# Performance work log

Measured on AMD Instinct MI355X. Metric: run time of the kernel, lower is better.

The kernel has to match this reference:

```python
import jax, jax.numpy as jnp
import numpy as np

B, T = 2048, 200
UC, IC, CC = 100000, 100000, 1000
UD, ID, CD = 128, 64, 64
K = ID + CD                      # keys_dim = item_dim + cate_dim = 128
D_JOIN = UD + K + K              # user_emb + item_join_emb + hist_hid_emb
D1, D2 = 80, 40                  # dim_layers[:-1]
BN_EPS = 1e-3                    # keras BatchNormalization default epsilon
MASK_VAL = -2.0**32 + 1.0


def _bn_train(x, gamma, beta):
    # keras BatchNorm, training mode (batch statistics over axis 0)
    m = jnp.mean(x, axis=0)
    v = jnp.var(x, axis=0)
    return (x - m) * jax.lax.rsqrt(v + BN_EPS) * gamma + beta


def _dice(x, alpha, beta):
    # dice: BN(center=False, scale=False) then learned soft gating
    m = jnp.mean(x, axis=0)
    v = jnp.var(x, axis=0)
    xn = (x - m) * jax.lax.rsqrt(v + BN_EPS)
    p = jax.nn.sigmoid(beta * xn)
    return alpha * (1.0 - p) * x + p * x


def setup_inputs() -> dict:
    key = jax.random.key(0)
    ks = jax.random.split(key, 32)
    f = jnp.float32
    inp = {
        "user": jax.random.randint(ks[0], (B,), 0, UC, dtype=jnp.int32),
        "item": jax.random.randint(ks[1], (B,), 0, IC, dtype=jnp.int32),
        "history": jax.random.randint(ks[2], (B, T), 0, IC, dtype=jnp.int32),
        "length": jax.random.randint(ks[3], (B,), 1, T + 1, dtype=jnp.int32),
        "cate_list": jax.random.randint(ks[4], (IC,), 0, CC, dtype=jnp.int32),
        # embedding tables + item bias
        "user_table": jax.random.normal(ks[5], (UC, UD), f) * 0.05,
        "item_table": jax.random.normal(ks[6], (IC, ID), f) * 0.05,
        "cate_table": jax.random.normal(ks[7], (CC, CD), f) * 0.05,
        "item_bias": jax.random.normal(ks[8], (IC,), f) * 0.01,
        # attention MLP: 4K -> 80 -> 40 -> 1 (sigmoid, sigmoid, linear)
        "att_W1": jax.random.normal(ks[9], (4 * K, D1), f) * 0.05,
        "att_b1": jnp.zeros((D1,), f),
        "att_W2": jax.random.normal(ks[10], (D1, D2), f) * 0.1,
        "att_b2": jnp.zeros((D2,), f),
        "att_W3": jax.random.normal(ks[11], (D2, 1), f) * 0.1,
        "att_b3": jnp.zeros((1,), f),
        # hist_bn + hist_fc (K -> K)
        "hbn_gamma": jnp.ones((K,), f),
        "hbn_beta": jnp.zeros((K,), f),
        "hist_W": jax.random.normal(ks[12], (K, K), f) * 0.05,
        "hist_b": jnp.zeros((K,), f),
        # final MLP: BN -> Dense(80)+dice -> Dense(40)+dice -> Dense(1)
        "fbn_gamma": jnp.ones((D_JOIN,), f),
        "fbn_beta": jnp.zeros((D_JOIN,), f),
        "fc1_W": jax.random.normal(ks[13], (D_JOIN, D1), f) * 0.05,
        "fc1_b": jnp.zeros((D1,), f),
        "d1_alpha": jax.random.normal(ks[14], (D1,), f) * 0.1,
        "d1_beta": jax.random.normal(ks[15], (D1,), f) * 0.1,
        "fc2_W": jax.random.normal(ks[16], (D1, D2), f) * 0.1,
        "fc2_b": jnp.zeros((D2,), f),
        "d2_alpha": jax.random.normal(ks[17], (D2,), f) * 0.1,
        "d2_beta": jax.random.normal(ks[18], (D2,), f) * 0.1,
        "fc3_W": jax.random.normal(ks[19], (D2, 1), f) * 0.1,
        "fc3_b": jnp.zeros((1,), f),
    }
    return inp


def reference(user, item, history, length, cate_list,
              user_table, item_table, cate_table, item_bias,
              att_W1, att_b1, att_W2, att_b2, att_W3, att_b3,
              hbn_gamma, hbn_beta, hist_W, hist_b,
              fbn_gamma, fbn_beta,
              fc1_W, fc1_b, d1_alpha, d1_beta,
              fc2_W, fc2_b, d2_alpha, d2_beta,
              fc3_W, fc3_b):
    # --- get_emb ---
    user_emb = user_table[user]                                   # [B, UD]
    item_join = jnp.concatenate([item_table[item], cate_table[cate_list[item]]], -1)  # [B, K]
    bias = item_bias[item]                                        # [B]
    hist_join = jnp.concatenate([item_table[history], cate_table[cate_list[history]]], -1)  # [B, T, K]

    # --- DIN attention ---
    q = jnp.broadcast_to(item_join[:, None, :], hist_join.shape)  # [B, T, K]
    din_all = jnp.concatenate([q, hist_join, q - hist_join, q * hist_join], -1)  # [B, T, 4K]
    h = jax.nn.sigmoid(din_all @ att_W1 + att_b1)
    h = jax.nn.sigmoid(h @ att_W2 + att_b2)
    scores = (h @ att_W3 + att_b3)[..., 0]                        # [B, T]
    mask = jnp.arange(T) < length[:, None]                        # [B, T]
    scores = jnp.where(mask, scores, MASK_VAL)
    scores = scores / (K ** 0.5)
    attn = jax.nn.softmax(scores, axis=-1)                        # [B, T]
    hist_attn = jnp.einsum('bt,btk->bk', attn, hist_join)         # [B, K]

    # --- hist_bn + hist_fc ---
    hist_hid = _bn_train(hist_attn, hbn_gamma, hbn_beta) @ hist_W + hist_b  # [B, K]

    # --- final MLP with dice ---
    join = jnp.concatenate([user_emb, item_join, hist_hid], -1)   # [B, D_JOIN]
    x = _bn_train(join, fbn_gamma, fbn_beta)
    x = _dice(x @ fc1_W + fc1_b, d1_alpha, d1_beta)
    x = _dice(x @ fc2_W + fc2_b, d2_alpha, d2_beta)
    output = (x @ fc3_W + fc3_b)[:, 0] + bias                     # [B]
    logit = jax.nn.sigmoid(output)
    return output, logit
```

## Files before the change

kernel.cpp:

```cpp
#include <hip/hip_runtime.h>
#include <math.h>

#define BB 2048
#define TT 200
#define BN_EPS 1e-3f
#define MASKV (-4294967295.0f)
#define INV_SQRTK 0.08838834764831845f

typedef short bfrag __attribute__((ext_vector_type(8)));
typedef float f32x4 __attribute__((ext_vector_type(4)));

__device__ __forceinline__ unsigned short f2b(float x) {
    union { float f; unsigned u; } v; v.f = x;
    unsigned r = (v.u + 0x7fffu + ((v.u >> 16) & 1u)) >> 16;
    return (unsigned short)r;
}
__device__ __forceinline__ float b2f(unsigned short u) {
    union { unsigned u; float f; } v; v.u = ((unsigned)u) << 16; return v.f;
}
__device__ __forceinline__ float sigm(float x) { return 1.f / (1.f + __expf(-x)); }

__global__ __launch_bounds__(256) void k0_prep(
    const float* __restrict__ W1, const float* __restrict__ fc1W,
    const float* __restrict__ fc2W, float* __restrict__ prep)
{
    const int gid = blockIdx.x * 256 + threadIdx.x;
    const int stride = gridDim.x * 256;
    float* W1bcT = prep;
    float* W1dT  = prep + 10240;
    float* W1ac  = prep + 20480;
    float* fc1WT = prep + 30720;
    float* fc2WT = prep + 61440;
    for (int i = gid; i < 10240; i += stride) {
        int j = i >> 7, k = i & 127;
        float wa = W1[k * 80 + j];
        float wb = W1[(128 + k) * 80 + j];
        float wc = W1[(256 + k) * 80 + j];
        float wd = W1[(384 + k) * 80 + j];
        W1bcT[i] = wb - wc;
        W1dT[i]  = wd;
        W1ac[k * 80 + j] = wa + wc;
    }
    for (int i = gid; i < 30720; i += stride) { int j = i / 384, c = i - j * 384; fc1WT[i] = fc1W[c * 80 + j]; }
    for (int i = gid; i < 3200;  i += stride) { int j = i / 80,  c = i - j * 80;  fc2WT[i] = fc2W[c * 40 + j]; }
}

__global__ __launch_bounds__(512) void k1_attn(
    const int* __restrict__ item, const int* __restrict__ history,
    const int* __restrict__ length, const int* __restrict__ cate_list,
    const float* __restrict__ item_table, const float* __restrict__ cate_table,
    const float* __restrict__ W1bcT, const float* __restrict__ W1dT,
    const float* __restrict__ W1ac,
    const float* __restrict__ b1, const float* __restrict__ W2,
    const float* __restrict__ b2, const float* __restrict__ W3,
    const float* __restrict__ b3,
    float* __restrict__ hist_attn, float* __restrict__ hstats)
{
    __shared__ unsigned short sA[208 * 136];
    __shared__ unsigned short sU[208 * 104];
    __shared__ unsigned short sW2[48 * 104];
    __shared__ float sQ[128], sCc[80], sCp[480], sPd[1024], sScore[256];
    __shared__ float sB2[48], sW3f[48];
    __shared__ int   sHist[TT], sCid[TT];
    __shared__ float sRed[8], sMS[2], sB3s;

    const int b   = blockIdx.x;
    const int tid = threadIdx.x;
    const int it  = item[b];
    const int len = length[b];

    if (tid < 64)       sQ[tid] = item_table[(size_t)it * 64 + tid];
    else if (tid < 128) sQ[tid] = cate_table[(size_t)cate_list[it] * 64 + (tid - 64)];
    if (tid < TT) { int h = history[(size_t)b * TT + tid]; sHist[tid] = h; sCid[tid] = cate_list[h]; }
    if (tid < 48) { sB2[tid] = (tid < 40) ? b2[tid] : 0.f; sW3f[tid] = (tid < 40) ? W3[tid] : 0.f; }
    if (tid < 256) sScore[tid] = 0.f;
    if (tid == 0) sB3s = b3[0];
    for (int i = tid; i < 8 * 136; i += 512) sA[200 * 136 + i] = 0;
    for (int i = tid; i < 48 * 104; i += 512) {
        int n = i / 104, k = i - n * 104;
        float v = (n < 40 && k < 80) ? W2[k * 40 + n] : 0.f;
        sW2[i] = f2b(v);
    }
    __syncthreads();

    for (int i = tid; i < 10240; i += 512) {
        int k = i & 127;
        sU[(i >> 7) * 136 + k] = f2b(W1bcT[i] + sQ[k] * W1dT[i]);
    }
    if (tid < 480) {
        int g = tid / 80, j = tid - g * 80;
        int kb = g * 22, ke = (kb + 22 < 128) ? kb + 22 : 128;
        float c = 0.f;
        for (int k = kb; k < ke; ++k) c = fmaf(sQ[k], W1ac[k * 80 + j], c);
        sCp[tid] = c;
    }
    for (int u = tid; u < 800; u += 512) {
        int r = u >> 2, s = u & 3;
        const float* src = (s < 2) ? (item_table + (size_t)sHist[r] * 64 + s * 32)
                                   : (cate_table + (size_t)sCid[r] * 64 + (s - 2) * 32);
        unsigned short* dst = &sA[r * 136 + s * 32];
#pragma unroll
        for (int q4 = 0; q4 < 8; ++q4) {
            float4 v = ((const float4*)src)[q4];
            ushort4 o; o.x = f2b(v.x); o.y = f2b(v.y); o.z = f2b(v.z); o.w = f2b(v.w);
            *(ushort4*)(dst + q4 * 4) = o;
        }
    }
    __syncthreads();

    if (tid < 80) {
        float c = b1[tid];
#pragma unroll
        for (int g = 0; g < 6; ++g) c += sCp[g * 80 + tid];
        sCc[tid] = c;
    }

    const int w = tid >> 6, l = tid & 63, lo16 = l & 15, hi = l >> 4;
    f32x4 accP[9];
#pragma unroll
    for (int pp = 0; pp < 9; ++pp) {
        int p = w + pp * 8;
        if (p < 65) {
            int mt = p / 5, nt = p - mt * 5;
            const unsigned short* Ab = &sA[(mt * 16 + lo16) * 136 + hi * 8];
            const unsigned short* Bb = &sU[(nt * 16 + lo16) * 136 + hi * 8];
            f32x4 acc = {0.f, 0.f, 0.f, 0.f};
#pragma unroll
            for (int ks = 0; ks < 4; ++ks) {
                bfrag a = *(const bfrag*)(Ab + ks * 32);
                bfrag bb = *(const bfrag*)(Bb + ks * 32);
                acc = __builtin_amdgcn_mfma_f32_16x16x32_bf16(a, bb, acc, 0, 0, 0);
            }
            accP[pp] = acc;
        }
    }
    __syncthreads();

#pragma unroll
    for (int pp = 0; pp < 9; ++pp) {
        int p = w + pp * 8;
        if (p < 65) {
            int mt = p / 5, nt = p - mt * 5;
            int j = nt * 16 + lo16;
            float cc = sCc[j];
#pragma unroll
            for (int rg = 0; rg < 4; ++rg) {
                int m = mt * 16 + hi * 4 + rg;
                sU[m * 104 + j] = f2b(sigm(accP[pp][rg] + cc));
            }
        }
    }
    for (int i = tid; i < 208 * 16; i += 512) {
        int r = i >> 4;
        sU[r * 104 + 80 + (i & 15)] = 0;
    }
    __syncthreads();

#pragma unroll
    for (int pp = 0; pp < 5; ++pp) {
        int p = w + pp * 8;
        if (p < 39) {
            int mt = p / 3, nt = p - mt * 3;
            const unsigned short* Ab = &sU[(mt * 16 + lo16) * 104 + hi * 8];
            const unsigned short* Bb = &sW2[(nt * 16 + lo16) * 104 + hi * 8];
            f32x4 acc = {0.f, 0.f, 0.f, 0.f};
#pragma unroll
            for (int ks = 0; ks < 3; ++ks) {
                bfrag a = *(const bfrag*)(Ab + ks * 32);
                bfrag bb = *(const bfrag*)(Bb + ks * 32);
                acc = __builtin_amdgcn_mfma_f32_16x16x32_bf16(a, bb, acc, 0, 0, 0);
            }
            int j2 = nt * 16 + lo16;
            float w3 = sW3f[j2], b2v = sB2[j2];
#pragma unroll
            for (int rg = 0; rg < 4; ++rg) {
                float pt = sigm(acc[rg] + b2v) * w3;
                pt += __shfl_xor(pt, 1);
                pt += __shfl_xor(pt, 2);
                pt += __shfl_xor(pt, 4);
                pt += __shfl_xor(pt, 8);
                if (lo16 == 0) atomicAdd(&sScore[mt * 16 + hi * 4 + rg], pt);
            }
        }
    }
    __syncthreads();

    int t = tid;
    float sc;
    if (t < TT) {
        float raw = sScore[t] + sB3s;
        if (t >= len) raw = MASKV;
        sc = raw * INV_SQRTK;
    } else {
        sc = -3.0e38f;
    }
    float mx = sc;
#pragma unroll
    for (int o = 32; o > 0; o >>= 1) mx = fmaxf(mx, __shfl_xor(mx, o));
    if ((tid & 63) == 0) sRed[tid >> 6] = mx;
    __syncthreads();
    if (tid == 0) {
        float m2 = sRed[0];
        for (int ww = 1; ww < 8; ++ww) m2 = fmaxf(m2, sRed[ww]);
        sMS[0] = m2;
    }
    __syncthreads();
    mx = sMS[0];
    float e = (t < TT) ? __expf(sc - mx) : 0.f;
    float sum = e;
#pragma unroll
    for (int o = 32; o > 0; o >>= 1) sum += __shfl_xor(sum, o);
    if ((tid & 63) == 0) sRed[tid >> 6] = sum;
    __syncthreads();
    if (tid == 0) {
        float s2 = 0.f;
        for (int ww = 0; ww < 8; ++ww) s2 += sRed[ww];
        sMS[1] = s2;
    }
    __syncthreads();
    float inv = 1.f / sMS[1];
    if (t < TT) sScore[t] = e * inv;
    __syncthreads();

    {
        const int k2 = (tid & 63) * 2;
        const int g  = tid >> 6;
        float a0 = 0.f, a1 = 0.f;
        for (int tt = g; tt < TT; tt += 8) {
            float aw = sScore[tt];
            unsigned pr = *(const unsigned*)&sA[tt * 136 + k2];
            a0 = fmaf(aw, b2f((unsigned short)(pr & 0xffffu)), a0);
            a1 = fmaf(aw, b2f((unsigned short)(pr >> 16)), a1);
        }
        sPd[g * 128 + k2]     = a0;
        sPd[g * 128 + k2 + 1] = a1;
    }
    __syncthreads();
    if (tid < 128) {
        float tot = 0.f;
#pragma unroll
        for (int g = 0; g < 8; ++g) tot += sPd[g * 128 + tid];
        hist_attn[(size_t)b * 128 + tid] = tot;
        atomicAdd(&hstats[tid], tot);
        atomicAdd(&hstats[128 + tid], tot * tot);
    }
}

__global__ __launch_bounds__(256) void k3_histfc_join(
    const float* __restrict__ hist_attn, const float* __restrict__ hstats,
    const float* __restrict__ hgamma, const float* __restrict__ hbeta,
    const float* __restrict__ histW, const float* __restrict__ histb,
    const int* __restrict__ user, const int* __restrict__ item,
    const int* __restrict__ cate_list,
    const float* __restrict__ user_table, const float* __restrict__ item_table,
    const float* __restrict__ cate_table,
    float* __restrict__ jbuf, float* __restrict__ jstats)
{
    __shared__ float sWs[128][132];
    __shared__ float sX[8][132];
    __shared__ float sCsP[2][128];
    __shared__ float sCb[128];
    __shared__ float sScale[128];
    __shared__ float sShift[128];

    const int tid = threadIdx.x;
    const int r0  = blockIdx.x * 8;
    if (tid < 128) {
        float m  = hstats[tid] * (1.f / 2048.f);
        float v  = hstats[128 + tid] * (1.f / 2048.f) - m * m;
        float rs = rsqrtf(v + BN_EPS);
        float scv = hgamma[tid] * rs;
        sScale[tid] = scv;
        sShift[tid] = hbeta[tid] - m * scv;
        sCb[tid] = histb[tid];
    }
    __syncthreads();
    for (int i = tid; i < 128 * 128; i += 256) {
        int k = i >> 7;
        sWs[k][i & 127] = sScale[k] * histW[i];
    }
    {
        int j = tid & 127, g = tid >> 7;
        float c = 0.f;
        for (int k = g * 64; k < g * 64 + 64; ++k) c = fmaf(sShift[k], histW[k * 128 + j], c);
        sCsP[g][j] = c;
    }
    for (int i = tid; i < 8 * 128; i += 256) {
        int r = i >> 7;
        sX[r][i & 127] = hist_attn[(size_t)(r0 + r) * 128 + (i & 127)];
    }
    __syncthreads();

    const int j  = tid & 127;
    const int rh = tid >> 7;
    float su0 = 0.f, su1 = 0.f, su2 = 0.f, sq0 = 0.f, sq1 = 0.f, sq2 = 0.f;
    for (int r = rh; r < 8; r += 2) {
        int row = r0 + r;
        float o = sCsP[0][j] + sCsP[1][j] + sCb[j];
        for (int k = 0; k < 128; ++k) o = fmaf(sX[r][k], sWs[k][j], o);
        int u    = user[row];
        float ue = user_table[(size_t)u * 128 + j];
        int itv  = item[row];
        float qv = (j < 64) ? item_table[(size_t)itv * 64 + j]
                            : cate_table[(size_t)cate_list[itv] * 64 + (j - 64)];
        jbuf[(size_t)row * 384 + j]       = ue;
        jbuf[(size_t)row * 384 + 128 + j] = qv;
        jbuf[(size_t)row * 384 + 256 + j] = o;
        su0 += ue; sq0 = fmaf(ue, ue, sq0);
        su1 += qv; sq1 = fmaf(qv, qv, sq1);
        su2 += o;  sq2 = fmaf(o, o, sq2);
    }
    atomicAdd(&jstats[j], su0);            atomicAdd(&jstats[384 + j], sq0);
    atomicAdd(&jstats[128 + j], su1);      atomicAdd(&jstats[384 + 128 + j], sq1);
    atomicAdd(&jstats[256 + j], su2);      atomicAdd(&jstats[384 + 256 + j], sq2);
}

__global__ __launch_bounds__(256) void k4_fc1(
    const float* __restrict__ jbuf, const float* __restrict__ jstats,
    const float* __restrict__ fgamma, const float* __restrict__ fbeta,
    const float* __restrict__ fc1WT, const float* __restrict__ fc1b,
    float* __restrict__ pre1, float* __restrict__ p1stats)
{
    __shared__ float sXn[8][388];
    __shared__ float sScale[384];
    __shared__ float sShift[384];
    const int tid = threadIdx.x;
    const int r0  = blockIdx.x * 8;
    for (int c = tid; c < 384; c += 256) {
        float m  = jstats[c] * (1.f / 2048.f);
        float v  = jstats[384 + c] * (1.f / 2048.f) - m * m;
        float rs = rsqrtf(v + BN_EPS);
        float scv = fgamma[c] * rs;
        sScale[c] = scv;
        sShift[c] = fbeta[c] - m * scv;
    }
    __syncthreads();
    for (int i = tid; i < 8 * 384; i += 256) {
        int r = i / 384, c = i - r * 384;
        sXn[r][c] = jbuf[(size_t)(r0 + r) * 384 + c] * sScale[c] + sShift[c];
    }
    __syncthreads();
    const int j1 = tid % 80;
    const int rg = tid / 80;
    if (rg < 3) {
        const float* wrow = fc1WT + (size_t)j1 * 384;
        float bias = fc1b[j1];
        float su = 0.f, sq = 0.f;
        for (int r = rg; r < 8; r += 3) {
            float a = bias;
            for (int c = 0; c < 384; c += 4) {
                float4 wv = *(const float4*)(wrow + c);
                float4 xv = *(const float4*)&sXn[r][c];
                a = fmaf(wv.x, xv.x, fmaf(wv.y, xv.y, fmaf(wv.z, xv.z, fmaf(wv.w, xv.w, a))));
            }
            pre1[(size_t)(r0 + r) * 80 + j1] = a;
            su += a;
            sq = fmaf(a, a, sq);
        }
        atomicAdd(&p1stats[j1], su);
        atomicAdd(&p1stats[80 + j1], sq);
    }
}

__global__ __launch_bounds__(256) void k5_fc2(
    const float* __restrict__ pre1, const float* __restrict__ p1stats,
    const float* __restrict__ d1a, const float* __restrict__ d1b,
    const float* __restrict__ fc2WT, const float* __restrict__ fc2b,
    float* __restrict__ pre2, float* __restrict__ p2stats)
{
    __shared__ float sX1[8][84];
    __shared__ float sM[80], sRs[80], sA[80], sBt[80];
    const int tid = threadIdx.x;
    const int r0  = blockIdx.x * 8;
    if (tid < 80) {
        float m = p1stats[tid] * (1.f / 2048.f);
        float v = p1stats[80 + tid] * (1.f / 2048.f) - m * m;
        sM[tid]  = m;
        sRs[tid] = rsqrtf(v + BN_EPS);
        sA[tid]  = d1a[tid];
        sBt[tid] = d1b[tid];
    }
    __syncthreads();
    for (int i = tid; i < 8 * 80; i += 256) {
        int r = i / 80, c = i - r * 80;
        float x  = pre1[(size_t)(r0 + r) * 80 + c];
        float xn = (x - sM[c]) * sRs[c];
        float p  = sigm(sBt[c] * xn);
        sX1[r][c] = x * (p + sA[c] * (1.f - p));
    }
    __syncthreads();
    const int j2 = tid % 40;
    const int rg = tid / 40;
    if (rg < 6) {
        const float* wrow = fc2WT + (size_t)j2 * 80;
        float bias = fc2b[j2];
        float su = 0.f, sq = 0.f;
        for (int r = rg; r < 8; r += 6) {
            float a = bias;
            for (int c = 0; c < 80; c += 4) {
                float4 wv = *(const float4*)(wrow + c);
                float4 xv = *(const float4*)&sX1[r][c];
                a = fmaf(wv.x, xv.x, fmaf(wv.y, xv.y, fmaf(wv.z, xv.z, fmaf(wv.w, xv.w, a))));
            }
            pre2[(size_t)(r0 + r) * 40 + j2] = a;
            su += a;
            sq = fmaf(a, a, sq);
        }
        atomicAdd(&p2stats[j2], su);
        atomicAdd(&p2stats[40 + j2], sq);
    }
}

__global__ __launch_bounds__(256) void k6_out(
    const float* __restrict__ pre2, const float* __restrict__ p2stats,
    const float* __restrict__ d2a, const float* __restrict__ d2b,
    const float* __restrict__ fc3W, const float* __restrict__ fc3b,
    const float* __restrict__ item_bias, const int* __restrict__ item,
    float* __restrict__ outp)
{
    __shared__ float sP[256 * 41];
    __shared__ float sM[40], sRs[40], sA[40], sBt[40], sW[40];
    __shared__ float sB3v;
    const int tid = threadIdx.x;
    const int r0  = blockIdx.x * 256;
    if (tid < 40) {
        float m = p2stats[tid] * (1.f / 2048.f);
        float v = p2stats[40 + tid] * (1.f / 2048.f) - m * m;
        sM[tid]  = m;
        sRs[tid] = rsqrtf(v + BN_EPS);
        sA[tid]  = d2a[tid];
        sBt[tid] = d2b[tid];
        sW[tid]  = fc3W[tid];
    }
    if (tid == 0) sB3v = fc3b[0];
    for (int i = tid; i < 256 * 40; i += 256) {
        int r = i / 40, c = i - r * 40;
        sP[r * 41 + c] = pre2[(size_t)(r0 + r) * 40 + c];
    }
    __syncthreads();
    const int r = r0 + tid;
    float a = sB3v;
    for (int c = 0; c < 40; ++c) {
        float x  = sP[tid * 41 + c];
        float xn = (x - sM[c]) * sRs[c];
        float p  = sigm(sBt[c] * xn);
        float x2 = x * (p + sA[c] * (1.f - p));
        a = fmaf(x2, sW[c], a);
    }
    a += item_bias[item[r]];
    outp[r]      = a;
    outp[BB + r] = sigm(a);
}

extern "C" void kernel_launch(void* const* d_in, const int* in_sizes, int n_in,
                              void* d_out, int out_size, void* d_ws, size_t ws_size,
                              hipStream_t stream)
{
    const int*   user       = (const int*)d_in[0];
    const int*   item       = (const int*)d_in[1];
    const int*   history    = (const int*)d_in[2];
    const int*   length     = (const int*)d_in[3];
    const int*   cate_list  = (const int*)d_in[4];
    const float* user_table = (const float*)d_in[5];
    const float* item_table = (const float*)d_in[6];
    const float* cate_table = (const float*)d_in[7];
    const float* item_bias  = (const float*)d_in[8];
    const float* att_W1 = (const float*)d_in[9];
    const float* att_b1 = (const float*)d_in[10];
    const float* att_W2 = (const float*)d_in[11];
    const float* att_b2 = (const float*)d_in[12];
    const float* att_W3 = (const float*)d_in[13];
    const float* att_b3 = (const float*)d_in[14];
    const float* hgam   = (const float*)d_in[15];
    const float* hbet   = (const float*)d_in[16];
    const float* histW  = (const float*)d_in[17];
    const float* histb  = (const float*)d_in[18];
    const float* fgam   = (const float*)d_in[19];
    const float* fbet   = (const float*)d_in[20];
    const float* fc1W   = (const float*)d_in[21];
    const float* fc1b   = (const float*)d_in[22];
    const float* d1a    = (const float*)d_in[23];
    const float* d1b    = (const float*)d_in[24];
    const float* fc2W   = (const float*)d_in[25];
    const float* fc2b   = (const float*)d_in[26];
    const float* d2a    = (const float*)d_in[27];
    const float* d2b    = (const float*)d_in[28];
    const float* fc3W   = (const float*)d_in[29];
    const float* fc3b   = (const float*)d_in[30];

    float* ws        = (float*)d_ws;
    float* hist_attn = ws;
    float* jbuf      = hist_attn + 262144;
    float* pre1      = jbuf + 786432;
    float* pre2      = pre1 + 163840;
    float* stats     = pre2 + 81920;
    float* hstats  = stats;
    float* jstats  = stats + 256;
    float* p1stats = jstats + 768;
    float* p2stats = p1stats + 160;
    float* prep    = stats + 1264;
    float* W1bcT = prep;
    float* W1dT  = prep + 10240;
    float* W1ac  = prep + 20480;
    float* fc1WT = prep + 30720;
    float* fc2WT = prep + 61440;

    hipMemsetAsync(stats, 0, 1264 * sizeof(float), stream);

    k0_prep<<<128, 256, 0, stream>>>(att_W1, fc1W, fc2W, prep);

    k1_attn<<<BB, 512, 0, stream>>>(item, history, length, cate_list,
        item_table, cate_table, W1bcT, W1dT, W1ac,
        att_b1, att_W2, att_b2, att_W3, att_b3,
        hist_attn, hstats);

    k3_histfc_join<<<256, 256, 0, stream>>>(hist_attn, hstats, hgam, hbet,
        histW, histb, user, item, cate_list, user_table, item_table, cate_table,
        jbuf, jstats);
    k4_fc1<<<256, 256, 0, stream>>>(jbuf, jstats, fgam, fbet, fc1WT, fc1b,
        pre1, p1stats);
    k5_fc2<<<256, 256, 0, stream>>>(pre1, p1stats, d1a, d1b, fc2WT, fc2b,
        pre2, p2stats);
    k6_out<<<8, 256, 0, stream>>>(pre2, p2stats, d2a, d2b, fc3W, fc3b,
        item_bias, item, (float*)d_out);
}
```

Measured before the change: 471.5 us.

## Halve attention LDS footprint via two-pass tiling and fuse tail MLP into cooperative kernel

The attention kernel now processes history in two 112-row passes with a smaller shared-memory footprint, keeps W2 fragments in registers, and sets launch bounds so four 512-thread blocks can be resident per CU. The weighted history sum re-reads fp32 embeddings from global memory instead of the bf16 LDS copy. The four tail kernels (hist fc, fc1, fc2, output) are merged into one cooperative kernel that uses grid syncs and keeps intermediates in shared memory, removing the global round trips. The costs are extra global gathers, grid-sync overhead, and a 256-block cooperative grid that must fit co-resident.

```diff
diff --git a/kernel.cpp b/kernel.cpp
--- a/kernel.cpp
+++ b/kernel.cpp
@@ -1,5 +1,8 @@
 #include <hip/hip_runtime.h>
+#include <hip/hip_cooperative_groups.h>
 #include <math.h>
+
+namespace cg = cooperative_groups;
 
 #define BB 2048
 #define TT 200
@@ -14,9 +17,6 @@
     union { float f; unsigned u; } v; v.f = x;
     unsigned r = (v.u + 0x7fffu + ((v.u >> 16) & 1u)) >> 16;
     return (unsigned short)r;
-}
-__device__ __forceinline__ float b2f(unsigned short u) {
-    union { unsigned u; float f; } v; v.u = ((unsigned)u) << 16; return v.f;
 }
 __device__ __forceinline__ float sigm(float x) { return 1.f / (1.f + __expf(-x)); }
 
@@ -26,79 +26,94 @@
 {
     const int gid = blockIdx.x * 256 + threadIdx.x;
     const int stride = gridDim.x * 256;
-    float* W1bcT = prep;
-    float* W1dT  = prep + 10240;
-    float* W1ac  = prep + 20480;
-    float* fc1WT = prep + 30720;
-    float* fc2WT = prep + 61440;
+    float* W1pair = prep;
+    float* W1ac   = prep + 20480;
+    float* fc1WT  = prep + 30720;
+    float* fc2WT  = prep + 61440;
     for (int i = gid; i < 10240; i += stride) {
         int j = i >> 7, k = i & 127;
         float wa = W1[k * 80 + j];
         float wb = W1[(128 + k) * 80 + j];
         float wc = W1[(256 + k) * 80 + j];
         float wd = W1[(384 + k) * 80 + j];
-        W1bcT[i] = wb - wc;
-        W1dT[i]  = wd;
-        W1ac[k * 80 + j] = wa + wc;
+        W1pair[i * 2]     = wb - wc;
+        W1pair[i * 2 + 1] = wd;
+        W1ac[k * 80 + j]  = wa + wc;
     }
     for (int i = gid; i < 30720; i += stride) { int j = i / 384, c = i - j * 384; fc1WT[i] = fc1W[c * 80 + j]; }
     for (int i = gid; i < 3200;  i += stride) { int j = i / 80,  c = i - j * 80;  fc2WT[i] = fc2W[c * 40 + j]; }
 }
 
-__global__ __launch_bounds__(512) void k1_attn(
+__global__ __launch_bounds__(512, 4) void k1_attn(
     const int* __restrict__ item, const int* __restrict__ history,
     const int* __restrict__ length, const int* __restrict__ cate_list,
     const float* __restrict__ item_table, const float* __restrict__ cate_table,
-    const float* __restrict__ W1bcT, const float* __restrict__ W1dT,
-    const float* __restrict__ W1ac,
+    const float* __restrict__ W1pair, const float* __restrict__ W1ac,
     const float* __restrict__ b1, const float* __restrict__ W2,
     const float* __restrict__ b2, const float* __restrict__ W3,
     const float* __restrict__ b3,
     float* __restrict__ hist_attn, float* __restrict__ hstats)
 {
-    __shared__ unsigned short sA[208 * 136];
-    __shared__ unsigned short sU[208 * 104];
-    __shared__ unsigned short sW2[48 * 104];
-    __shared__ float sQ[128], sCc[80], sCp[480], sPd[1024], sScore[256];
+    __shared__ __align__(16) unsigned short sA[112 * 136];
+    __shared__ __align__(16) unsigned short sW1[80 * 136];
+    __shared__ __align__(16) unsigned short sH1[112 * 104];
+    __shared__ float sScore[256];
+    __shared__ float sCc[80];
+    __shared__ int   sHist[TT], sCid[TT];
     __shared__ float sB2[48], sW3f[48];
-    __shared__ int   sHist[TT], sCid[TT];
-    __shared__ float sRed[8], sMS[2], sB3s;
+    __shared__ float sRed[8], sMS[2], sB3v;
+
+    float* const sQ  = sScore;
+    float* const sCp = (float*)sH1;
+    float* const sPd = (float*)sH1;
 
     const int b   = blockIdx.x;
     const int tid = threadIdx.x;
     const int it  = item[b];
     const int len = length[b];
+    const int w = tid >> 6, l = tid & 63, lo16 = l & 15, hi = l >> 4;
+
+    bfrag w2f[3][3];
+#pragma unroll
+    for (int nt = 0; nt < 3; ++nt)
+#pragma unroll
+        for (int ks = 0; ks < 3; ++ks) {
+            bfrag f;
+#pragma unroll
+            for (int i = 0; i < 8; ++i) {
+                int k = ks * 32 + hi * 8 + i, j2 = nt * 16 + lo16;
+                float v = (k < 80 && j2 < 40) ? W2[k * 40 + j2] : 0.f;
+                f[i] = (short)f2b(v);
+            }
+            w2f[nt][ks] = f;
+        }
 
     if (tid < 64)       sQ[tid] = item_table[(size_t)it * 64 + tid];
     else if (tid < 128) sQ[tid] = cate_table[(size_t)cate_list[it] * 64 + (tid - 64)];
     if (tid < TT) { int h = history[(size_t)b * TT + tid]; sHist[tid] = h; sCid[tid] = cate_list[h]; }
     if (tid < 48) { sB2[tid] = (tid < 40) ? b2[tid] : 0.f; sW3f[tid] = (tid < 40) ? W3[tid] : 0.f; }
-    if (tid < 256) sScore[tid] = 0.f;
-    if (tid == 0) sB3s = b3[0];
-    for (int i = tid; i < 8 * 136; i += 512) sA[200 * 136 + i] = 0;
-    for (int i = tid; i < 48 * 104; i += 512) {
-        int n = i / 104, k = i - n * 104;
-        float v = (n < 40 && k < 80) ? W2[k * 40 + n] : 0.f;
-        sW2[i] = f2b(v);
-    }
-    __syncthreads();
-
-    for (int i = tid; i < 10240; i += 512) {
-        int k = i & 127;
-        sU[(i >> 7) * 136 + k] = f2b(W1bcT[i] + sQ[k] * W1dT[i]);
+    if (tid == 0) sB3v = b3[0];
+    __syncthreads();
+
+    for (int i = tid; i < 5120; i += 512) {
+        int j = i >> 6, kh = (i & 63) * 2;
+        float4 p = *(const float4*)&W1pair[(size_t)(j * 128 + kh) * 2];
+        float2 q = *(const float2*)&sQ[kh];
+        unsigned pk = (unsigned)f2b(p.x + q.x * p.y) | ((unsigned)f2b(p.z + q.y * p.w) << 16);
+        *(unsigned*)&sW1[j * 136 + kh] = pk;
     }
     if (tid < 480) {
         int g = tid / 80, j = tid - g * 80;
-        int kb = g * 22, ke = (kb + 22 < 128) ? kb + 22 : 128;
+        int k0 = g * 22, k1e = (k0 + 22 < 128) ? k0 + 22 : 128;
         float c = 0.f;
-        for (int k = kb; k < ke; ++k) c = fmaf(sQ[k], W1ac[k * 80 + j], c);
+        for (int k = k0; k < k1e; ++k) c = fmaf(sQ[k], W1ac[k * 80 + j], c);
         sCp[tid] = c;
     }
-    for (int u = tid; u < 800; u += 512) {
-        int r = u >> 2, s = u & 3;
+    if (tid < 448) {
+        int r = tid >> 2, s = tid & 3;
+        unsigned short* dst = &sA[r * 136 + s * 32];
         const float* src = (s < 2) ? (item_table + (size_t)sHist[r] * 64 + s * 32)
                                    : (cate_table + (size_t)sCid[r] * 64 + (s - 2) * 32);
-        unsigned short* dst = &sA[r * 136 + s * 32];
 #pragma unroll
         for (int q4 = 0; q4 < 8; ++q4) {
             float4 v = ((const float4*)src)[q4];
@@ -114,62 +129,88 @@
         for (int g = 0; g < 6; ++g) c += sCp[g * 80 + tid];
         sCc[tid] = c;
     }
-
-    const int w = tid >> 6, l = tid & 63, lo16 = l & 15, hi = l >> 4;
-    f32x4 accP[9];
-#pragma unroll
-    for (int pp = 0; pp < 9; ++pp) {
+    if (tid < 256) sScore[tid] = 0.f;
+    __syncthreads();
+
+    f32x4 acc1[5];
+#pragma unroll
+    for (int pp = 0; pp < 5; ++pp) {
         int p = w + pp * 8;
-        if (p < 65) {
+        if (p < 35) {
             int mt = p / 5, nt = p - mt * 5;
             const unsigned short* Ab = &sA[(mt * 16 + lo16) * 136 + hi * 8];
-            const unsigned short* Bb = &sU[(nt * 16 + lo16) * 136 + hi * 8];
+            const unsigned short* Bb = &sW1[(nt * 16 + lo16) * 136 + hi * 8];
             f32x4 acc = {0.f, 0.f, 0.f, 0.f};
 #pragma unroll
-            for (int ks = 0; ks < 4; ++ks) {
-                bfrag a = *(const bfrag*)(Ab + ks * 32);
-                bfrag bb = *(const bfrag*)(Bb + ks * 32);
-                acc = __builtin_amdgcn_mfma_f32_16x16x32_bf16(a, bb, acc, 0, 0, 0);
-            }
-            accP[pp] = acc;
-        }
-    }
-    __syncthreads();
-
-#pragma unroll
-    for (int pp = 0; pp < 9; ++pp) {
+            for (int ks = 0; ks < 4; ++ks)
+                acc = __builtin_amdgcn_mfma_f32_16x16x32_bf16(
+                    *(const bfrag*)(Ab + ks * 32), *(const bfrag*)(Bb + ks * 32), acc, 0, 0, 0);
+            acc1[pp] = acc;
+        }
+    }
+    __syncthreads();
+
+#pragma unroll
+    for (int pp = 0; pp < 5; ++pp) {
         int p = w + pp * 8;
-        if (p < 65) {
+        if (p < 35) {
             int mt = p / 5, nt = p - mt * 5;
             int j = nt * 16 + lo16;
             float cc = sCc[j];
 #pragma unroll
-            for (int rg = 0; rg < 4; ++rg) {
-                int m = mt * 16 + hi * 4 + rg;
-                sU[m * 104 + j] = f2b(sigm(accP[pp][rg] + cc));
+            for (int rg = 0; rg < 4; ++rg)
+                sH1[(mt * 16 + hi * 4 + rg) * 104 + j] = f2b(sigm(acc1[pp][rg] + cc));
+        }
+    }
+    for (int i = tid; i < 112 * 16; i += 512) sH1[(i >> 4) * 104 + 80 + (i & 15)] = 0;
+    if (tid < 448) {
+        int r = tid >> 2, s = tid & 3;
+        int t = 112 + r;
+        unsigned short* dst = &sA[r * 136 + s * 32];
+        if (t < TT) {
+            const float* src = (s < 2) ? (item_table + (size_t)sHist[t] * 64 + s * 32)
+                                       : (cate_table + (size_t)sCid[t] * 64 + (s - 2) * 32);
+#pragma unroll
+            for (int q4 = 0; q4 < 8; ++q4) {
+                float4 v = ((const float4*)src)[q4];
+                ushort4 o; o.x = f2b(v.x); o.y = f2b(v.y); o.z = f2b(v.z); o.w = f2b(v.w);
+                *(ushort4*)(dst + q4 * 4) = o;
             }
-        }
-    }
-    for (int i = tid; i < 208 * 16; i += 512) {
-        int r = i >> 4;
-        sU[r * 104 + 80 + (i & 15)] = 0;
-    }
-    __syncthreads();
-
+        } else {
+            ushort4 z = {0, 0, 0, 0};
+#pragma unroll
+            for (int q4 = 0; q4 < 8; ++q4) *(ushort4*)(dst + q4 * 4) = z;
+        }
+    }
+    __syncthreads();
+
+    f32x4 acc2[5];
 #pragma unroll
     for (int pp = 0; pp < 5; ++pp) {
         int p = w + pp * 8;
-        if (p < 39) {
+        if (p < 35) {
+            int mt = p / 5, nt = p - mt * 5;
+            const unsigned short* Ab = &sA[(mt * 16 + lo16) * 136 + hi * 8];
+            const unsigned short* Bb = &sW1[(nt * 16 + lo16) * 136 + hi * 8];
+            f32x4 acc = {0.f, 0.f, 0.f, 0.f};
+#pragma unroll
+            for (int ks = 0; ks < 4; ++ks)
+                acc = __builtin_amdgcn_mfma_f32_16x16x32_bf16(
+                    *(const bfrag*)(Ab + ks * 32), *(const bfrag*)(Bb + ks * 32), acc, 0, 0, 0);
+            acc2[pp] = acc;
+        }
+    }
+#pragma unroll
+    for (int pp = 0; pp < 3; ++pp) {
+        int p = w + pp * 8;
+        if (p < 21) {
             int mt = p / 3, nt = p - mt * 3;
-            const unsigned short* Ab = &sU[(mt * 16 + lo16) * 104 + hi * 8];
-            const unsigned short* Bb = &sW2[(nt * 16 + lo16) * 104 + hi * 8];
+            const unsigned short* Ab = &sH1[(mt * 16 + lo16) * 104 + hi * 8];
             f32x4 acc = {0.f, 0.f, 0.f, 0.f};
 #pragma unroll
-            for (int ks = 0; ks < 3; ++ks) {
-                bfrag a = *(const bfrag*)(Ab + ks * 32);
-                bfrag bb = *(const bfrag*)(Bb + ks * 32);
-                acc = __builtin_amdgcn_mfma_f32_16x16x32_bf16(a, bb, acc, 0, 0, 0);
-            }
+            for (int ks = 0; ks < 3; ++ks)
+                acc = __builtin_amdgcn_mfma_f32_16x16x32_bf16(
+                    *(const bfrag*)(Ab + ks * 32), w2f[nt][ks], acc, 0, 0, 0);
             int j2 = nt * 16 + lo16;
             float w3 = sW3f[j2], b2v = sB2[j2];
 #pragma unroll
@@ -185,10 +226,50 @@
     }
     __syncthreads();
 
+#pragma unroll
+    for (int pp = 0; pp < 5; ++pp) {
+        int p = w + pp * 8;
+        if (p < 35) {
+            int mt = p / 5, nt = p - mt * 5;
+            int j = nt * 16 + lo16;
+            float cc = sCc[j];
+#pragma unroll
+            for (int rg = 0; rg < 4; ++rg)
+                sH1[(mt * 16 + hi * 4 + rg) * 104 + j] = f2b(sigm(acc2[pp][rg] + cc));
+        }
+    }
+    __syncthreads();
+
+#pragma unroll
+    for (int pp = 0; pp < 3; ++pp) {
+        int p = w + pp * 8;
+        if (p < 21) {
+            int mt = p / 3, nt = p - mt * 3;
+            const unsigned short* Ab = &sH1[(mt * 16 + lo16) * 104 + hi * 8];
+            f32x4 acc = {0.f, 0.f, 0.f, 0.f};
+#pragma unroll
+            for (int ks = 0; ks < 3; ++ks)
+                acc = __builtin_amdgcn_mfma_f32_16x16x32_bf16(
+                    *(const bfrag*)(Ab + ks * 32), w2f[nt][ks], acc, 0, 0, 0);
+            int j2 = nt * 16 + lo16;
+            float w3 = sW3f[j2], b2v = sB2[j2];
+#pragma unroll
+            for (int rg = 0; rg < 4; ++rg) {
+                float pt = sigm(acc[rg] + b2v) * w3;
+                pt += __shfl_xor(pt, 1);
+                pt += __shfl_xor(pt, 2);
+                pt += __shfl_xor(pt, 4);
+                pt += __shfl_xor(pt, 8);
+                if (lo16 == 0) atomicAdd(&sScore[112 + mt * 16 + hi * 4 + rg], pt);
+            }
+        }
+    }
+    __syncthreads();
+
     int t = tid;
     float sc;
     if (t < TT) {
-        float raw = sScore[t] + sB3s;
+        float raw = sScore[t] + sB3v;
         if (t >= len) raw = MASKV;
         sc = raw * INV_SQRTK;
     } else {
@@ -223,233 +304,229 @@
     __syncthreads();
 
     {
-        const int k2 = (tid & 63) * 2;
-        const int g  = tid >> 6;
-        float a0 = 0.f, a1 = 0.f;
-        for (int tt = g; tt < TT; tt += 8) {
+        const int rg = tid >> 5, c4 = tid & 31;
+        f32x4 ad = {0.f, 0.f, 0.f, 0.f};
+        for (int tt = rg; tt < TT; tt += 16) {
             float aw = sScore[tt];
-            unsigned pr = *(const unsigned*)&sA[tt * 136 + k2];
-            a0 = fmaf(aw, b2f((unsigned short)(pr & 0xffffu)), a0);
-            a1 = fmaf(aw, b2f((unsigned short)(pr >> 16)), a1);
-        }
-        sPd[g * 128 + k2]     = a0;
-        sPd[g * 128 + k2 + 1] = a1;
+            const float* p = (c4 < 16) ? (item_table + (size_t)sHist[tt] * 64 + c4 * 4)
+                                       : (cate_table + (size_t)sCid[tt] * 64 + (c4 - 16) * 4);
+            float4 v = *(const float4*)p;
+            ad[0] = fmaf(aw, v.x, ad[0]);
+            ad[1] = fmaf(aw, v.y, ad[1]);
+            ad[2] = fmaf(aw, v.z, ad[2]);
+            ad[3] = fmaf(aw, v.w, ad[3]);
+        }
+        *(f32x4*)&sPd[rg * 128 + c4 * 4] = ad;
     }
     __syncthreads();
     if (tid < 128) {
         float tot = 0.f;
 #pragma unroll
-        for (int g = 0; g < 8; ++g) tot += sPd[g * 128 + tid];
+        for (int g = 0; g < 16; ++g) tot += sPd[g * 128 + tid];
         hist_attn[(size_t)b * 128 + tid] = tot;
         atomicAdd(&hstats[tid], tot);
         atomicAdd(&hstats[128 + tid], tot * tot);
     }
 }
 
-__global__ __launch_bounds__(256) void k3_histfc_join(
-    const float* __restrict__ hist_attn, const float* __restrict__ hstats,
-    const float* __restrict__ hgamma, const float* __restrict__ hbeta,
-    const float* __restrict__ histW, const float* __restrict__ histb,
-    const int* __restrict__ user, const int* __restrict__ item,
-    const int* __restrict__ cate_list,
-    const float* __restrict__ user_table, const float* __restrict__ item_table,
-    const float* __restrict__ cate_table,
-    float* __restrict__ jbuf, float* __restrict__ jstats)
+struct TailArgs {
+    const float *hist_attn, *hstats;
+    const float *hgamma, *hbeta, *histW, *histb;
+    const int *user, *item, *cate_list;
+    const float *user_table, *item_table, *cate_table;
+    float *jstats, *p1stats, *p2stats;
+    const float *fgamma, *fbeta, *fc1WT, *fc1b, *d1a, *d1b;
+    const float *fc2WT, *fc2b, *d2a, *d2b, *fc3W, *fc3b, *item_bias;
+    float *outp;
+};
+
+__global__ __launch_bounds__(256) void k_tail(TailArgs a)
 {
-    __shared__ float sWs[128][132];
-    __shared__ float sX[8][132];
-    __shared__ float sCsP[2][128];
-    __shared__ float sCb[128];
-    __shared__ float sScale[128];
-    __shared__ float sShift[128];
+    cg::grid_group grid = cg::this_grid();
+
+    __shared__ float sWs[128 * 132];
+    __shared__ float sJoin[8 * 388];
+    __shared__ float sX[8 * 132];
+    __shared__ float sScaleH[128], sShiftH[128], sCsP[2][128], sCb[128];
+    __shared__ float sScaleJ[384], sShiftJ[384];
+    __shared__ float sPre1[8 * 84];
+    __shared__ float sPre2[8 * 44];
+    __shared__ float sM1[80], sRs1[80], sA1[80], sBt1[80];
+    __shared__ float sM2[40], sRs2[40], sA2[40], sBt2[40], sW3t[40];
+    __shared__ float sB3t;
+
+    float* const sXn = sWs;
+    float* const sX1 = sX;
 
     const int tid = threadIdx.x;
     const int r0  = blockIdx.x * 8;
+
     if (tid < 128) {
-        float m  = hstats[tid] * (1.f / 2048.f);
-        float v  = hstats[128 + tid] * (1.f / 2048.f) - m * m;
+        float m  = a.hstats[tid] * (1.f / 2048.f);
+        float v  = a.hstats[128 + tid] * (1.f / 2048.f) - m * m;
         float rs = rsqrtf(v + BN_EPS);
-        float scv = hgamma[tid] * rs;
-        sScale[tid] = scv;
-        sShift[tid] = hbeta[tid] - m * scv;
-        sCb[tid] = histb[tid];
+        float scv = a.hgamma[tid] * rs;
+        sScaleH[tid] = scv;
+        sShiftH[tid] = a.hbeta[tid] - m * scv;
+        sCb[tid] = a.histb[tid];
     }
     __syncthreads();
     for (int i = tid; i < 128 * 128; i += 256) {
         int k = i >> 7;
-        sWs[k][i & 127] = sScale[k] * histW[i];
+        sWs[k * 132 + (i & 127)] = sScaleH[k] * a.histW[i];
     }
     {
         int j = tid & 127, g = tid >> 7;
         float c = 0.f;
-        for (int k = g * 64; k < g * 64 + 64; ++k) c = fmaf(sShift[k], histW[k * 128 + j], c);
+        for (int k = g * 64; k < g * 64 + 64; ++k) c = fmaf(sShiftH[k], a.histW[k * 128 + j], c);
         sCsP[g][j] = c;
     }
     for (int i = tid; i < 8 * 128; i += 256) {
         int r = i >> 7;
-        sX[r][i & 127] = hist_attn[(size_t)(r0 + r) * 128 + (i & 127)];
-    }
-    __syncthreads();
-
-    const int j  = tid & 127;
-    const int rh = tid >> 7;
-    float su0 = 0.f, su1 = 0.f, su2 = 0.f, sq0 = 0.f, sq1 = 0.f, sq2 = 0.f;
-    for (int r = rh; r < 8; r += 2) {
-        int row = r0 + r;
-        float o = sCsP[0][j] + sCsP[1][j] + sCb[j];
-        for (int k = 0; k < 128; ++k) o = fmaf(sX[r][k], sWs[k][j], o);
-        int u    = user[row];
-        float ue = user_table[(size_t)u * 128 + j];
-        int itv  = item[row];
-        float qv = (j < 64) ? item_table[(size_t)itv * 64 + j]
-                            : cate_table[(size_t)cate_list[itv] * 64 + (j - 64)];
-        jbuf[(size_t)row * 384 + j]       = ue;
-        jbuf[(size_t)row * 384 + 128 + j] = qv;
-        jbuf[(size_t)row * 384 + 256 + j] = o;
-        su0 += ue; sq0 = fmaf(ue, ue, sq0);
-        su1 += qv; sq1 = fmaf(qv, qv, sq1);
-        su2 += o;  sq2 = fmaf(o, o, sq2);
-    }
-    atomicAdd(&jstats[j], su0);            atomicAdd(&jstats[384 + j], sq0);
-    atomicAdd(&jstats[128 + j], su1);      atomicAdd(&jstats[384 + 128 + j], sq1);
-    atomicAdd(&jstats[256 + j], su2);      atomicAdd(&jstats[384 + 256 + j], sq2);
-}
-
-__global__ __launch_bounds__(256) void k4_fc1(
-    const float* __restrict__ jbuf, const float* __restrict__ jstats,
-    const float* __restrict__ fgamma, const float* __restrict__ fbeta,
-    const float* __restrict__ fc1WT, const float* __restrict__ fc1b,
-    float* __restrict__ pre1, float* __restrict__ p1stats)
-{
-    __shared__ float sXn[8][388];
-    __shared__ float sScale[384];
-    __shared__ float sShift[384];
-    const int tid = threadIdx.x;
-    const int r0  = blockIdx.x * 8;
+        sX[r * 132 + (i & 127)] = a.hist_attn[(size_t)(r0 + r) * 128 + (i & 127)];
+    }
+    __syncthreads();
+    {
+        const int j  = tid & 127;
+        const int rh = tid >> 7;
+        float su0 = 0.f, su1 = 0.f, su2 = 0.f, sq0 = 0.f, sq1 = 0.f, sq2 = 0.f;
+        for (int r = rh; r < 8; r += 2) {
+            int row = r0 + r;
+            float o = sCsP[0][j] + sCsP[1][j] + sCb[j];
+            for (int k = 0; k < 128; ++k) o = fmaf(sX[r * 132 + k], sWs[k * 132 + j], o);
+            float ue = a.user_table[(size_t)a.user[row] * 128 + j];
+            int itv  = a.item[row];
+            float qv = (j < 64) ? a.item_table[(size_t)itv * 64 + j]
+                                : a.cate_table[(size_t)a.cate_list[itv] * 64 + (j - 64)];
+            sJoin[r * 388 + j]       = ue;
+            sJoin[r * 388 + 128 + j] = qv;
+            sJoin[r * 388 + 256 + j] = o;
+            su0 += ue; sq0 = fmaf(ue, ue, sq0);
+            su1 += qv; sq1 = fmaf(qv, qv, sq1);
+            su2 += o;  sq2 = fmaf(o, o, sq2);
+        }
+        atomicAdd(&a.jstats[j], su0);       atomicAdd(&a.jstats[384 + j], sq0);
+        atomicAdd(&a.jstats[128 + j], su1); atomicAdd(&a.jstats[384 + 128 + j], sq1);
+        atomicAdd(&a.jstats[256 + j], su2); atomicAdd(&a.jstats[384 + 256 + j], sq2);
+    }
+    grid.sync();
+
     for (int c = tid; c < 384; c += 256) {
-        float m  = jstats[c] * (1.f / 2048.f);
-        float v  = jstats[384 + c] * (1.f / 2048.f) - m * m;
+        float m  = a.jstats[c] * (1.f / 2048.f);
+        float v  = a.jstats[384 + c] * (1.f / 2048.f) - m * m;
         float rs = rsqrtf(v + BN_EPS);
-        float scv = fgamma[c] * rs;
-        sScale[c] = scv;
-        sShift[c] = fbeta[c] - m * scv;
+        float scv = a.fgamma[c] * rs;
+        sScaleJ[c] = scv;
+        sShiftJ[c] = a.fbeta[c] - m * scv;
     }
     __syncthreads();
     for (int i = tid; i < 8 * 384; i += 256) {
         int r = i / 384, c = i - r * 384;
-        sXn[r][c] = jbuf[(size_t)(r0 + r) * 384 + c] * sScale[c] + sShift[c];
-    }
-    __syncthreads();
-    const int j1 = tid % 80;
-    const int rg = tid / 80;
-    if (rg < 3) {
-        const float* wrow = fc1WT + (size_t)j1 * 384;
-        float bias = fc1b[j1];
-        float su = 0.f, sq = 0.f;
-        for (int r = rg; r < 8; r += 3) {
-            float a = bias;
-            for (int c = 0; c < 384; c += 4) {
-                float4 wv = *(const float4*)(wrow + c);
-                float4 xv = *(const float4*)&sXn[r][c];
-                a = fmaf(wv.x, xv.x, fmaf(wv.y, xv.y, fmaf(wv.z, xv.z, fmaf(wv.w, xv.w, a))));
+        sXn[r * 388 + c] = sJoin[r * 388 + c] * sScaleJ[c] + sShiftJ[c];
+    }
+    __syncthreads();
+    {
+        const int j1 = tid % 80;
+        const int rg = tid / 80;
+        if (rg < 3) {
+            const float* wrow = a.fc1WT + (size_t)j1 * 384;
+            float bias = a.fc1b[j1];
+            float su = 0.f, sq = 0.f;
+            for (int r = rg; r < 8; r += 3) {
+                float acc = bias;
+                for (int c = 0; c < 384; c += 4) {
+                    float4 wv = *(const float4*)(wrow + c);
+                    float4 xv = *(const float4*)&sXn[r * 388 + c];
+                    acc = fmaf(wv.x, xv.x, fmaf(wv.y, xv.y, fmaf(wv.z, xv.z, fmaf(wv.w, xv.w, acc))));
+                }
+                sPre1[r * 84 + j1] = acc;
+                su += acc;
+                sq = fmaf(acc, acc, sq);
             }
-            pre1[(size_t)(r0 + r) * 80 + j1] = a;
-            su += a;
-            sq = fmaf(a, a, sq);
-        }
-        atomicAdd(&p1stats[j1], su);
-        atomicAdd(&p1stats[80 + j1], sq);
-    }
-}
-
-__global__ __launch_bounds__(256) void k5_fc2(
-    const float* __restrict__ pre1, const float* __restrict__ p1stats,
-    const float* __restrict__ d1a, const float* __restrict__ d1b,
-    const float* __restrict__ fc2WT, const float* __restrict__ fc2b,
-    float* __restrict__ pre2, float* __restrict__ p2stats)
-{
-    __shared__ float sX1[8][84];
-    __shared__ float sM[80], sRs[80], sA[80], sBt[80];
-    const int tid = threadIdx.x;
-    const int r0  = blockIdx.x * 8;
+            atomicAdd(&a.p1stats[j1], su);
+            atomicAdd(&a.p1stats[80 + j1], sq);
+        }
+    }
+    grid.sync();
+
     if (tid < 80) {
-        float m = p1stats[tid] * (1.f / 2048.f);
-        float v = p1stats[80 + tid] * (1.f / 2048.f) - m * m;
-        sM[tid]  = m;
-        sRs[tid] = rsqrtf(v + BN_EPS);
-        sA[tid]  = d1a[tid];
-        sBt[tid] = d1b[tid];
+        float m = a.p1stats[tid] * (1.f / 2048.f);
+        float v = a.p1stats[80 + tid] * (1.f / 2048.f) - m * m;
+        sM1[tid]  = m;
+        sRs1[tid] = rsqrtf(v + BN_EPS);
+        sA1[tid]  = a.d1a[tid];
+        sBt1[tid] = a.d1b[tid];
     }
     __syncthreads();
     for (int i = tid; i < 8 * 80; i += 256) {
         int r = i / 80, c = i - r * 80;
-        float x  = pre1[(size_t)(r0 + r) * 80 + c];
-        float xn = (x - sM[c]) * sRs[c];
-        float p  = sigm(sBt[c] * xn);
-        sX1[r][c] = x * (p + sA[c] * (1.f - p));
-    }
-    __syncthreads();
-    const int j2 = tid % 40;
-    const int rg = tid / 40;
-    if (rg < 6) {
-        const float* wrow = fc2WT + (size_t)j2 * 80;
-        float bias = fc2b[j2];
-        float su = 0.f, sq = 0.f;
-        for (int r = rg; r < 8; r += 6) {
-            float a = bias;
-            for (int c = 0; c < 80; c += 4) {
-                float4 wv = *(const float4*)(wrow + c);
-                float4 xv = *(const float4*)&sX1[r][c];
-                a = fmaf(wv.x, xv.x, fmaf(wv.y, xv.y, fmaf(wv.z, xv.z, fmaf(wv.w, xv.w, a))));
+        float x  = sPre1[r * 84 + c];
+        float xn = (x - sM1[c]) * sRs1[c];
+        float p  = sigm(sBt1[c] * xn);
+        sX1[r * 84 + c] = x * (p + sA1[c] * (1.f - p));
+    }
+    __syncthreads();
+    {
+        const int j2 = tid % 40;
+        const int rg = tid / 40;
+        if (rg < 6) {
+            const float* wrow = a.fc2WT + (size_t)j2 * 80;
+            float bias = a.fc2b[j2];
+            float su = 0.f, sq = 0.f;
+            for (int r = rg; r < 8; r += 6) {
+                float acc = bias;
+                for (int c = 0; c < 80; c += 4) {
+                    float4 wv = *(const float4*)(wrow + c);
+                    float4 xv = *(const float4*)&sX1[r * 84 + c];
+                    acc = fmaf(wv.x, xv.x, fmaf(wv.y, xv.y, fmaf(wv.z, xv.z, fmaf(wv.w, xv.w, acc))));
+                }
+                sPre2[r * 44 + j2] = acc;
+                su += acc;
+                sq = fmaf(acc, acc, sq);
             }
-            pre2[(size_t)(r0 + r) * 40 + j2] = a;
-            su += a;
-            sq = fmaf(a, a, sq);
-        }
-        atomicAdd(&p2stats[j2], su);
-        atomicAdd(&p2stats[40 + j2], sq);
-    }
-}
-
-__global__ __launch_bounds__(256) void k6_out(
-    const float* __restrict__ pre2, const float* __restrict__ p2stats,
-    const float* __restrict__ d2a, const float* __restrict__ d2b,
-    const float* __restrict__ fc3W, const float* __restrict__ fc3b,
-    const float* __restrict__ item_bias, const int* __restrict__ item,
-    float* __restrict__ outp)
-{
-    __shared__ float sP[256 * 41];
-    __shared__ float sM[40], sRs[40], sA[40], sBt[40], sW[40];
-    __shared__ float sB3v;
-    const int tid = threadIdx.x;
-    const int r0  = blockIdx.x * 256;
+            atomicAdd(&a.p2stats[j2], su);
+            atomicAdd(&a.p2stats[40 + j2], sq);
+        }
+    }
+    grid.sync();
+
     if (tid < 40) {
-        float m = p2stats[tid] * (1.f / 2048.f);
-        float v = p2stats[40 + tid] * (1.f / 2048.f) - m * m;
-        sM[tid]  = m;
-        sRs[tid] = rsqrtf(v + BN_EPS);
-        sA[tid]  = d2a[tid];
-        sBt[tid] = d2b[tid];
-        sW[tid]  = fc3W[tid];
-    }
-    if (tid == 0) sB3v = fc3b[0];
-    for (int i = tid; i < 256 * 40; i += 256) {
-        int r = i / 40, c = i - r * 40;
-        sP[r * 41 + c] = pre2[(size_t)(r0 + r) * 40 + c];
-    }
-    __syncthreads();
-    const int r = r0 + tid;
-    float a = sB3v;
-    for (int c = 0; c < 40; ++c) {
-        float x  = sP[tid * 41 + c];
-        float xn = (x - sM[c]) * sRs[c];
-        float p  = sigm(sBt[c] * xn);
-        float x2 = x * (p + sA[c] * (1.f - p));
-        a = fmaf(x2, sW[c], a);
-    }
-    a += item_bias[item[r]];
-    outp[r]      = a;
-    outp[BB + r] = sigm(a);
+        float m = a.p2stats[tid] * (1.f / 2048.f);
+        float v = a.p2stats[40 + tid] * (1.f / 2048.f) - m * m;
+        sM2[tid]  = m;
+        sRs2[tid] = rsqrtf(v + BN_EPS);
+        sA2[tid]  = a.d2a[tid];
+        sBt2[tid] = a.d2b[tid];
+        sW3t[tid] = a.fc3W[tid];
+    }
+    if (tid == 0) sB3t = a.fc3b[0];
+    __syncthreads();
+    {
+        const int r = tid >> 5, lane = tid & 31;
+        float part = 0.f;
+        int c = lane;
+        {
+            float x  = sPre2[r * 44 + c];
+            float xn = (x - sM2[c]) * sRs2[c];
+            float p  = sigm(sBt2[c] * xn);
+            part = fmaf(x * (p + sA2[c] * (1.f - p)), sW3t[c], part);
+        }
+        if (lane < 8) {
+            int c2 = lane + 32;
+            float x  = sPre2[r * 44 + c2];
+            float xn = (x - sM2[c2]) * sRs2[c2];
+            float p  = sigm(sBt2[c2] * xn);
+            part = fmaf(x * (p + sA2[c2] * (1.f - p)), sW3t[c2], part);
+        }
+#pragma unroll
+        for (int o = 16; o > 0; o >>= 1) part += __shfl_xor(part, o);
+        if (lane == 0) {
+            int row = r0 + r;
+            float v = part + sB3t + a.item_bias[a.item[row]];
+            a.outp[row]      = v;
+            a.outp[BB + row] = sigm(v);
+        }
+    }
 }
 
 extern "C" void kernel_launch(void* const* d_in, const int* in_sizes, int n_in,
@@ -490,37 +567,37 @@
 
     float* ws        = (float*)d_ws;
     float* hist_attn = ws;
-    float* jbuf      = hist_attn + 262144;
-    float* pre1      = jbuf + 786432;
-    float* pre2      = pre1 + 163840;
-    float* stats     = pre2 + 81920;
+    float* stats     = hist_attn + 262144;
     float* hstats  = stats;
     float* jstats  = stats + 256;
     float* p1stats = jstats + 768;
     float* p2stats = p1stats + 160;
     float* prep    = stats + 1264;
-    float* W1bcT = prep;
-    float* W1dT  = prep + 10240;
-    float* W1ac  = prep + 20480;
-    float* fc1WT = prep + 30720;
-    float* fc2WT = prep + 61440;
+    float* W1pair = prep;
+    float* W1ac   = prep + 20480;
+    float* fc1WT  = prep + 30720;
+    float* fc2WT  = prep + 61440;
 
     hipMemsetAsync(stats, 0, 1264 * sizeof(float), stream);
 
     k0_prep<<<128, 256, 0, stream>>>(att_W1, fc1W, fc2W, prep);
 
     k1_attn<<<BB, 512, 0, stream>>>(item, history, length, cate_list,
-        item_table, cate_table, W1bcT, W1dT, W1ac,
+        item_table, cate_table, W1pair, W1ac,
         att_b1, att_W2, att_b2, att_W3, att_b3,
         hist_attn, hstats);
 
-    k3_histfc_join<<<256, 256, 0, stream>>>(hist_attn, hstats, hgam, hbet,
-        histW, histb, user, item, cate_list, user_table, item_table, cate_table,
-        jbuf, jstats);
-    k4_fc1<<<256, 256, 0, stream>>>(jbuf, jstats, fgam, fbet, fc1WT, fc1b,
-        pre1, p1stats);
-    k5_fc2<<<256, 256, 0, stream>>>(pre1, p1stats, d1a, d1b, fc2WT, fc2b,
-        pre2, p2stats);
-    k6_out<<<8, 256, 0, stream>>>(pre2, p2stats, d2a, d2b, fc3W, fc3b,
-        item_bias, item, (float*)d_out);
+    TailArgs ta;
+    ta.hist_attn = hist_attn; ta.hstats = hstats;
+    ta.hgamma = hgam; ta.hbeta = hbet; ta.histW = histW; ta.histb = histb;
+    ta.user = user; ta.item = item; ta.cate_list = cate_list;
+    ta.user_table = user_table; ta.item_table = item_table; ta.cate_table = cate_table;
+    ta.jstats = jstats; ta.p1stats = p1stats; ta.p2stats = p2stats;
+    ta.fgamma = fgam; ta.fbeta = fbet; ta.fc1WT = fc1WT; ta.fc1b = fc1b;
+    ta.d1a = d1a; ta.d1b = d1b; ta.fc2WT = fc2WT; ta.fc2b = fc2b;
+    ta.d2a = d2a; ta.d2b = d2b; ta.fc3W = fc3W; ta.fc3b = fc3b;
+    ta.item_bias = item_bias; ta.outp = (float*)d_out;
+
+    void* kargs[] = { &ta };
+    hipLaunchCooperativeKernel((void*)k_tail, dim3(256), dim3(256), kargs, 0, stream);
 }
```

After: 561.5 us. 1.19x slower.
